# Kernel optimization log

Measured on AMD Instinct MI355X. Metric: run time of the kernel, lower is better.

The kernel has to match this reference:

```python
import jax, jax.numpy as jnp
import numpy as np


def _step(state):
    # state: [B, H, W] in {0.0, 1.0}
    p = jnp.pad(state, ((0, 0), (1, 1), (1, 1)))
    neighbors = (p[:, :-2, :-2] + p[:, :-2, 1:-1] + p[:, :-2, 2:]
                 + p[:, 1:-1, :-2] + p[:, 1:-1, 2:]
                 + p[:, 2:, :-2] + p[:, 2:, 1:-1] + p[:, 2:, 2:])
    alive = state > 0.5
    survives = alive & ((neighbors == 2.0) | (neighbors == 3.0))
    born = (~alive) & (neighbors == 3.0)
    return jnp.where(survives | born, jnp.ones_like(state), jnp.zeros_like(state))


def setup_inputs() -> dict:
    key = jax.random.key(0)
    k1, k2 = jax.random.split(key)
    B, H, W = 32, 1024, 1024
    # Binary occupancy grids in {0.0, 1.0} as the rule expects
    initial_state = (jax.random.uniform(k1, (B, H, W)) > 0.5).astype(jnp.float32)
    target = (jax.random.uniform(k2, (B, H, W)) > 0.5).astype(jnp.float32)
    return {"initial_state": initial_state, "target": target, "generations": 8}


def reference(initial_state, target, generations):
    state = initial_state
    for _ in range(generations):  # small fixed unroll, strict sequential dependency
        state = _step(state)
    error = state - target
    loss = jnp.mean(error * error)
    live_cells = state.sum()
    max_abs_error = jnp.abs(error).max()
    return loss, state, target, live_cells, max_abs_error
```

## Files before the change

kernel.cpp:

```cpp
#include <hip/hip_runtime.h>
#include <cstdint>

typedef unsigned long long u64;
typedef float f4v __attribute__((ext_vector_type(4)));

#define BATCH   32
#define H       1024
#define W       1024
#define WPR     16
#define GENS    8
#define HALO    8
#define NTOT    33554432ULL
#define NROWS   (BATCH * H)

__device__ __forceinline__ u64 shflxor64(u64 v, int m) {
    return (u64)__shfl_xor((long long)v, m, 64);
}

#define PK_THREADS 256
#define PK_WAVES   4
#define PK_RPB     16
#define PK_GRID    (NROWS / PK_RPB)

__global__ __launch_bounds__(PK_THREADS)
void gol_pack(const float* __restrict__ in_state, u64* __restrict__ packed)
{
    const int tid  = threadIdx.x;
    const int wave = tid >> 6;
    const int lane = tid & 63;
    const int sub  = lane & 15;
    const int wsub = lane >> 4;

    const int row0 = blockIdx.x * PK_RPB;
    #pragma unroll
    for (int rr = 0; rr < PK_RPB / PK_WAVES; ++rr) {
        int row = row0 + wave + rr * PK_WAVES;
        const f4v* rowp4 = (const f4v*)(in_state + (size_t)row * W);
        u64* prow = packed + (size_t)row * WPR;
        #pragma unroll
        for (int g = 0; g < 4; ++g) {
            f4v f = rowp4[g * 64 + lane];
            u64 nib = (u64)((f.x > 0.5f) | ((f.y > 0.5f) << 1) |
                            ((f.z > 0.5f) << 2) | ((f.w > 0.5f) << 3));
            u64 v = nib << (sub * 4);
            v |= shflxor64(v, 1);
            v |= shflxor64(v, 2);
            v |= shflxor64(v, 4);
            v |= shflxor64(v, 8);
            if (sub == 0)
                prow[g * 4 + wsub] = v;
        }
    }
}

#define TR      32
#define BR      (TR + 2*HALO)
#define BRP     (BR + 2)
#define WP      (WPR + 2)
#define LF_THREADS 256
#define LF_GRID (BATCH * (H / TR))

__global__ __launch_bounds__(LF_THREADS)
void gol_life(const u64* __restrict__ packedI, u64* __restrict__ packedO)
{
    __shared__ u64 buf[2][BRP][WP];

    const int tile = blockIdx.x;
    const int tpb  = H / TR;
    const int b    = tile / tpb;
    const int r0   = (tile - b * tpb) * TR;

    const int tid  = threadIdx.x;

    for (int i = tid; i < 2 * BRP * WP; i += LF_THREADS)
        ((u64*)buf)[i] = 0ULL;
    __syncthreads();

    const u64* packedb = packedI + (size_t)b * H * WPR;
    #pragma unroll
    for (int k = 0; k < (BR * WPR) / LF_THREADS; ++k) {
        int idx = tid + k * LF_THREADS;
        int br = idx >> 4;
        int c  = idx & 15;
        int gr = r0 - HALO + br;
        if (gr >= 0 && gr < H)
            buf[0][br + 1][c + 1] = packedb[(size_t)gr * WPR + c];
    }
    __syncthreads();

    int cur = 0;
    for (int step = 0; step < GENS; ++step) {
        #pragma unroll
        for (int k = 0; k < (BR * WPR) / LF_THREADS; ++k) {
            int idx = tid + k * LF_THREADS;
            int br = idx >> 4;
            int c  = (idx & 15) + 1;
            int r  = br + 1;
            int gr = r0 - HALO + br;

            u64 uL = buf[cur][r-1][c-1], uC = buf[cur][r-1][c], uR = buf[cur][r-1][c+1];
            u64 mL = buf[cur][r  ][c-1], mC = buf[cur][r  ][c], mR = buf[cur][r  ][c+1];
            u64 dL = buf[cur][r+1][c-1], dC = buf[cur][r+1][c], dR = buf[cur][r+1][c+1];

            u64 uw = (uC << 1) | (uL >> 63), ue = (uC >> 1) | (uR << 63);
            u64 mw = (mC << 1) | (mL >> 63), me = (mC >> 1) | (mR << 63);
            u64 dw = (dC << 1) | (dL >> 63), de = (dC >> 1) | (dR << 63);
            u64 o0 = uw ^ uC ^ ue, t0 = (uw & uC) | (ue & (uw ^ uC));
            u64 o1 = mw ^ mC ^ me, t1 = (mw & mC) | (me & (mw ^ mC));
            u64 o2 = dw ^ dC ^ de, t2 = (dw & dC) | (de & (dw ^ dC));

            u64 oa = o0 ^ o1 ^ o2;
            u64 oc = (o0 & o1) | (o2 & (o0 ^ o1));
            u64 ts = t0 ^ t1 ^ t2;
            u64 tc = (t0 & t1) | (t2 & (t0 ^ t1));
            u64 b1 = oc ^ ts;
            u64 cc = oc & ts;
            u64 b2 = cc ^ tc;
            u64 b3 = cc & tc;
            u64 eq3 = oa & b1 & ~(b2 | b3);
            u64 eq4 = (~oa) & (~b1) & b2 & (~b3);
            u64 nxtw = eq3 | (mC & eq4);

            buf[cur ^ 1][r][c] = (gr >= 0 && gr < H) ? nxtw : 0ULL;
        }
        __syncthreads();
        cur ^= 1;
    }

    const size_t Rbase = (size_t)b * H + r0;
    #pragma unroll
    for (int k = 0; k < (TR * WPR) / LF_THREADS; ++k) {
        int idx = tid + k * LF_THREADS;
        int lr = idx >> 4;
        int c  = idx & 15;
        packedO[(Rbase + lr) * WPR + c] = buf[cur][HALO + lr + 1][c + 1];
    }
}

#define UP_THREADS 256
#define UP_WAVES   4
#define UP_RPB     8
#define UP_GRID    (NROWS / UP_RPB)
#define NSLOTS     (UP_GRID * UP_WAVES)

__global__ __launch_bounds__(UP_THREADS)
void gol_unpack(const u64* __restrict__ packedS,
                const float* __restrict__ target,
                float* __restrict__ out,
                u64* __restrict__ slots)
{
    const int tid  = threadIdx.x;
    const int wave = tid >> 6;
    const int lane = tid & 63;
    const int R0   = blockIdx.x * UP_RPB;

    float* o_state = out + 1;
    float* o_tgt   = out + 1 + NTOT;

    unsigned int mism = 0, live = 0;
    #pragma unroll
    for (int rr = 0; rr < UP_RPB / UP_WAVES; ++rr) {
        int row = R0 + wave + rr * UP_WAVES;
        size_t rowbase = (size_t)row * W;
        const u64* wrow = packedS + (size_t)row * WPR;
        const float* trow = target + rowbase;
        float* osrow = o_state + rowbase;
        float* otrow = o_tgt + rowbase;
        #pragma unroll
        for (int g = 0; g < 4; ++g) {
            int k = g * 64 + lane;
            if (k < 255) {
                int bitbase = 4 * k + 3;
                int w0 = bitbase >> 6;
                int sh = bitbase & 63;
                u64 lo = wrow[w0];
                u64 hi = wrow[w0 + 1];
                unsigned bits = (unsigned)(((lo >> sh) | (hi << (64 - sh))) & 0xFULL);
                f4v t = *(const f4v*)(trow + bitbase);
                unsigned tb = (unsigned)((t.x > 0.5f) | ((t.y > 0.5f) << 1) |
                                         ((t.z > 0.5f) << 2) | ((t.w > 0.5f) << 3));
                mism += (unsigned)__popc(bits ^ tb);
                live += (unsigned)__popc(bits);
                f4v sv;
                sv.x = (float)(bits & 1u);
                sv.y = (float)((bits >> 1) & 1u);
                sv.z = (float)((bits >> 2) & 1u);
                sv.w = (float)((bits >> 3) & 1u);
                *(f4v*)(osrow + bitbase) = sv;
                *(f4v*)(otrow + bitbase) = t;
            } else {
                u64 wfirst = wrow[0];
                u64 wlast  = wrow[15];
                unsigned hb   = (unsigned)(wfirst & 7ULL);
                unsigned tbit = (unsigned)(wlast >> 63);
                float t0 = trow[0], t1 = trow[1], t2 = trow[2], t3 = trow[1023];
                unsigned htb = (unsigned)((t0 > 0.5f) | ((t1 > 0.5f) << 1) | ((t2 > 0.5f) << 2));
                unsigned ttb = (unsigned)(t3 > 0.5f);
                mism += (unsigned)__popc(hb ^ htb) + (tbit ^ ttb);
                live += (unsigned)__popc(hb) + tbit;
                osrow[0] = (float)(hb & 1u);
                osrow[1] = (float)((hb >> 1) & 1u);
                osrow[2] = (float)((hb >> 2) & 1u);
                osrow[1023] = (float)tbit;
                otrow[0] = t0; otrow[1] = t1; otrow[2] = t2; otrow[1023] = t3;
            }
        }
    }

    u64 comb = ((u64)mism << 32) | (u64)live;
    #pragma unroll
    for (int m = 1; m < 64; m <<= 1)
        comb += (u64)__shfl_xor((long long)comb, m, 64);
    if (lane == 0)
        slots[blockIdx.x * UP_WAVES + wave] = comb;
}

__global__ __launch_bounds__(256)
void gol_finalize(const u64* __restrict__ slots, float* __restrict__ out)
{
    __shared__ u64 wsum[4];
    const int tid  = threadIdx.x;
    const int wave = tid >> 6;
    const int lane = tid & 63;

    u64 s = 0;
    for (int i = tid; i < NSLOTS; i += 256)
        s += slots[i];
    #pragma unroll
    for (int m = 1; m < 64; m <<= 1)
        s += (u64)__shfl_xor((long long)s, m, 64);
    if (lane == 0) wsum[wave] = s;
    __syncthreads();
    if (tid == 0) {
        u64 tot = wsum[0] + wsum[1] + wsum[2] + wsum[3];
        unsigned int mism = (unsigned int)(tot >> 32);
        unsigned int live = (unsigned int)(tot & 0xFFFFFFFFULL);
        out[0]            = (float)((double)mism / (double)NTOT);
        out[1 + 2*NTOT]   = (float)live;
        out[2 + 2*NTOT]   = (mism > 0) ? 1.0f : 0.0f;
    }
}

extern "C" void kernel_launch(void* const* d_in, const int* in_sizes, int n_in,
                              void* d_out, int out_size, void* d_ws, size_t ws_size,
                              hipStream_t stream) {
    (void)in_sizes; (void)n_in; (void)out_size; (void)ws_size;
    const float* in_state = (const float*)d_in[0];
    const float* target   = (const float*)d_in[1];
    float* out = (float*)d_out;

    u64* slots   = (u64*)d_ws;
    u64* packedI = (u64*)((char*)d_ws + (1u << 20));
    u64* packedO = (u64*)((char*)d_ws + (6u << 20));

    gol_pack    <<<dim3(PK_GRID), dim3(PK_THREADS), 0, stream>>>(in_state, packedI);
    gol_life    <<<dim3(LF_GRID), dim3(LF_THREADS), 0, stream>>>(packedI, packedO);
    gol_unpack  <<<dim3(UP_GRID), dim3(UP_THREADS), 0, stream>>>(packedO, target, out, slots);
    gol_finalize<<<1, 256, 0, stream>>>(slots, out);
}
```

Baseline: 494.5 us.

## Bit-pack target and fuse loss reductions into the life kernel

```diff
diff --git a/kernel.cpp b/kernel.cpp
--- a/kernel.cpp
+++ b/kernel.cpp
@@ -23,7 +23,10 @@
 #define PK_GRID    (NROWS / PK_RPB)
 
 __global__ __launch_bounds__(PK_THREADS)
-void gol_pack(const float* __restrict__ in_state, u64* __restrict__ packed)
+void gol_pack2(const float* __restrict__ in_state,
+               const float* __restrict__ target,
+               u64* __restrict__ packedI,
+               u64* __restrict__ packedT)
 {
     const int tid  = threadIdx.x;
     const int wave = tid >> 6;
@@ -31,12 +34,17 @@
     const int sub  = lane & 15;
     const int wsub = lane >> 4;
 
-    const int row0 = blockIdx.x * PK_RPB;
+    const int isT  = (blockIdx.x >= PK_GRID);
+    const float* src = isT ? target  : in_state;
+    u64*         dst = isT ? packedT : packedI;
+    const int blk  = isT ? (blockIdx.x - PK_GRID) : blockIdx.x;
+
+    const int row0 = blk * PK_RPB;
     #pragma unroll
     for (int rr = 0; rr < PK_RPB / PK_WAVES; ++rr) {
         int row = row0 + wave + rr * PK_WAVES;
-        const f4v* rowp4 = (const f4v*)(in_state + (size_t)row * W);
-        u64* prow = packed + (size_t)row * WPR;
+        const f4v* rowp4 = (const f4v*)(src + (size_t)row * W);
+        u64* prow = dst + (size_t)row * WPR;
         #pragma unroll
         for (int g = 0; g < 4; ++g) {
             f4v f = rowp4[g * 64 + lane];
@@ -58,10 +66,15 @@
 #define BRP     (BR + 2)
 #define WP      (WPR + 2)
 #define LF_THREADS 256
+#define LF_WAVES   4
 #define LF_GRID (BATCH * (H / TR))
+#define NSLOTS  (LF_GRID * LF_WAVES)
 
 __global__ __launch_bounds__(LF_THREADS)
-void gol_life(const u64* __restrict__ packedI, u64* __restrict__ packedO)
+void gol_life(const u64* __restrict__ packedI,
+              const u64* __restrict__ packedT,
+              u64* __restrict__ packedO,
+              u64* __restrict__ slots)
 {
     __shared__ u64 buf[2][BRP][WP];
 
@@ -71,6 +84,8 @@
     const int r0   = (tile - b * tpb) * TR;
 
     const int tid  = threadIdx.x;
+    const int wave = tid >> 6;
+    const int lane = tid & 63;
 
     for (int i = tid; i < 2 * BRP * WP; i += LF_THREADS)
         ((u64*)buf)[i] = 0ULL;
@@ -128,26 +143,35 @@
     }
 
     const size_t Rbase = (size_t)b * H + r0;
+    unsigned int mism = 0, live = 0;
     #pragma unroll
     for (int k = 0; k < (TR * WPR) / LF_THREADS; ++k) {
         int idx = tid + k * LF_THREADS;
         int lr = idx >> 4;
         int c  = idx & 15;
-        packedO[(Rbase + lr) * WPR + c] = buf[cur][HALO + lr + 1][c + 1];
-    }
+        u64 s = buf[cur][HALO + lr + 1][c + 1];
+        u64 t = packedT[(Rbase + lr) * WPR + c];
+        packedO[(Rbase + lr) * WPR + c] = s;
+        mism += (unsigned)__popcll(s ^ t);
+        live += (unsigned)__popcll(s);
+    }
+
+    u64 comb = ((u64)mism << 32) | (u64)live;
+    #pragma unroll
+    for (int m = 1; m < 64; m <<= 1)
+        comb += (u64)__shfl_xor((long long)comb, m, 64);
+    if (lane == 0)
+        slots[blockIdx.x * LF_WAVES + wave] = comb;
 }
 
 #define UP_THREADS 256
 #define UP_WAVES   4
 #define UP_RPB     8
 #define UP_GRID    (NROWS / UP_RPB)
-#define NSLOTS     (UP_GRID * UP_WAVES)
 
 __global__ __launch_bounds__(UP_THREADS)
-void gol_unpack(const u64* __restrict__ packedS,
-                const float* __restrict__ target,
-                float* __restrict__ out,
-                u64* __restrict__ slots)
+void gol_unpack_state(const u64* __restrict__ packedS,
+                      float* __restrict__ out)
 {
     const int tid  = threadIdx.x;
     const int wave = tid >> 6;
@@ -155,17 +179,13 @@
     const int R0   = blockIdx.x * UP_RPB;
 
     float* o_state = out + 1;
-    float* o_tgt   = out + 1 + NTOT;
-
-    unsigned int mism = 0, live = 0;
+
     #pragma unroll
     for (int rr = 0; rr < UP_RPB / UP_WAVES; ++rr) {
         int row = R0 + wave + rr * UP_WAVES;
         size_t rowbase = (size_t)row * W;
         const u64* wrow = packedS + (size_t)row * WPR;
-        const float* trow = target + rowbase;
         float* osrow = o_state + rowbase;
-        float* otrow = o_tgt + rowbase;
         #pragma unroll
         for (int g = 0; g < 4; ++g) {
             int k = g * 64 + lane;
@@ -176,43 +196,24 @@
                 u64 lo = wrow[w0];
                 u64 hi = wrow[w0 + 1];
                 unsigned bits = (unsigned)(((lo >> sh) | (hi << (64 - sh))) & 0xFULL);
-                f4v t = *(const f4v*)(trow + bitbase);
-                unsigned tb = (unsigned)((t.x > 0.5f) | ((t.y > 0.5f) << 1) |
-                                         ((t.z > 0.5f) << 2) | ((t.w > 0.5f) << 3));
-                mism += (unsigned)__popc(bits ^ tb);
-                live += (unsigned)__popc(bits);
                 f4v sv;
                 sv.x = (float)(bits & 1u);
                 sv.y = (float)((bits >> 1) & 1u);
                 sv.z = (float)((bits >> 2) & 1u);
                 sv.w = (float)((bits >> 3) & 1u);
                 *(f4v*)(osrow + bitbase) = sv;
-                *(f4v*)(otrow + bitbase) = t;
             } else {
                 u64 wfirst = wrow[0];
                 u64 wlast  = wrow[15];
                 unsigned hb   = (unsigned)(wfirst & 7ULL);
                 unsigned tbit = (unsigned)(wlast >> 63);
-                float t0 = trow[0], t1 = trow[1], t2 = trow[2], t3 = trow[1023];
-                unsigned htb = (unsigned)((t0 > 0.5f) | ((t1 > 0.5f) << 1) | ((t2 > 0.5f) << 2));
-                unsigned ttb = (unsigned)(t3 > 0.5f);
-                mism += (unsigned)__popc(hb ^ htb) + (tbit ^ ttb);
-                live += (unsigned)__popc(hb) + tbit;
                 osrow[0] = (float)(hb & 1u);
                 osrow[1] = (float)((hb >> 1) & 1u);
                 osrow[2] = (float)((hb >> 2) & 1u);
                 osrow[1023] = (float)tbit;
-                otrow[0] = t0; otrow[1] = t1; otrow[2] = t2; otrow[1023] = t3;
             }
         }
     }
-
-    u64 comb = ((u64)mism << 32) | (u64)live;
-    #pragma unroll
-    for (int m = 1; m < 64; m <<= 1)
-        comb += (u64)__shfl_xor((long long)comb, m, 64);
-    if (lane == 0)
-        slots[blockIdx.x * UP_WAVES + wave] = comb;
 }
 
 __global__ __launch_bounds__(256)
@@ -252,9 +253,12 @@
     u64* slots   = (u64*)d_ws;
     u64* packedI = (u64*)((char*)d_ws + (1u << 20));
     u64* packedO = (u64*)((char*)d_ws + (6u << 20));
-
-    gol_pack    <<<dim3(PK_GRID), dim3(PK_THREADS), 0, stream>>>(in_state, packedI);
-    gol_life    <<<dim3(LF_GRID), dim3(LF_THREADS), 0, stream>>>(packedI, packedO);
-    gol_unpack  <<<dim3(UP_GRID), dim3(UP_THREADS), 0, stream>>>(packedO, target, out, slots);
+    u64* packedT = (u64*)((char*)d_ws + (11u << 20));
+
+    gol_pack2<<<dim3(2 * PK_GRID), dim3(PK_THREADS), 0, stream>>>(in_state, target, packedI, packedT);
+    gol_life<<<dim3(LF_GRID), dim3(LF_THREADS), 0, stream>>>(packedI, packedT, packedO, slots);
+    gol_unpack_state<<<dim3(UP_GRID), dim3(UP_THREADS), 0, stream>>>(packedO, out);
+    hipMemcpyAsync(out + 1 + NTOT, target, NTOT * sizeof(float),
+                   hipMemcpyDeviceToDevice, stream);
     gol_finalize<<<1, 256, 0, stream>>>(slots, out);
 }
```

After: 558.9 us. +13.0%, slower.
